# Kernel optimization log

Hardware: AMD Instinct MI355X
Metric: run time of the kernel (lower is better)

## Reference

```python
import jax, jax.numpy as jnp
import numpy as np

C = 1024            # hidden_dim // compression_rate
IN_DIM = 1024
OUT_DIM = 1024
FFT_LEN = C // 2 + 1
CURV = 1e-4         # self.c
EPS = 1e-7
LN_EPS = 1e-5


def _mobius_scalar_mul(r, x, c):
    # r (x) x = tanh(r * atanh(sqrt(c)||x||)) * x / (sqrt(c)||x||)
    sqrt_c = jnp.sqrt(c)
    norm = jnp.maximum(jnp.linalg.norm(x, axis=-1, keepdims=True), EPS)
    scn = jnp.clip(sqrt_c * norm, EPS, 1.0 - 1e-5)
    return jnp.tanh(r * jnp.arctanh(scn)) * x / (sqrt_c * norm)


def _mobius_add(x, y, c):
    x2 = jnp.sum(x * x, axis=-1, keepdims=True)
    y2 = jnp.sum(y * y, axis=-1, keepdims=True)
    xy = jnp.sum(x * y, axis=-1, keepdims=True)
    num = (1.0 + 2.0 * c * xy + c * y2) * x + (1.0 - c * x2) * y
    den = 1.0 + 2.0 * c * xy + (c * c) * x2 * y2
    return num / jnp.maximum(den, EPS)


def _poincare_ball_layer(u, v, c, t):
    # geodesic-style interpolation: ((1-t) (x) u) (+) (t (x) v)
    return _mobius_add(_mobius_scalar_mul(1.0 - t, u, c),
                       _mobius_scalar_mul(t, v, c), c)


def setup_inputs() -> dict:
    key = jax.random.key(0)
    k_x, k_p, k_d = jax.random.split(key, 3)
    std = 0.02
    x = jax.random.normal(k_x, (4, 2048, IN_DIM), dtype=jnp.float32)
    proj_w = jax.random.normal(k_p, (C, IN_DIM), dtype=jnp.float32) * std
    freq_w = jnp.zeros((FFT_LEN,), dtype=jnp.float32)
    t = jnp.float32(0.3)
    ln_g = jnp.ones((C,), dtype=jnp.float32)
    ln_b = jnp.zeros((C,), dtype=jnp.float32)
    down_w = jax.random.normal(k_d, (OUT_DIM, C), dtype=jnp.float32) * std
    scale = jnp.float32(1.0)
    return {"x": x, "proj_w": proj_w, "ln_g": ln_g, "ln_b": ln_b,
            "freq_w": freq_w, "t": t, "down_w": down_w, "scale": scale}


def reference(x, proj_w, ln_g, ln_b, freq_w, t, down_w, scale):
    B, L, _ = x.shape
    # non-sep branch (hidden_dim > in_dim): silu(Linear(x))
    comp = jax.nn.silu(jnp.einsum('bli,ci->blc', x, proj_w))
    mu = jnp.mean(comp, axis=-1, keepdims=True)
    var = jnp.var(comp, axis=-1, keepdims=True)
    comp = (comp - mu) * jax.lax.rsqrt(var + LN_EPS) * ln_g + ln_b
    comp = comp.reshape(-1, C)                     # [B*L, C]
    Xf = jnp.fft.rfft(comp, axis=1)                # [B*L, C//2+1]
    w = jax.nn.softmax(freq_w)[None, :]
    flat = jnp.fft.irfft(Xf * w, n=C, axis=1)
    flat = jnp.nan_to_num(flat)
    shift = jnp.nan_to_num(t * flat)
    hyp = jnp.nan_to_num(_poincare_ball_layer(flat, shift, CURV, t))
    hyp = hyp.reshape(B, L, C)
    return jnp.einsum('blc,oc->blo', hyp, down_w) * scale
```

## Files before the change

kernel.cpp:

```cpp
#include <hip/hip_runtime.h>
#include <math.h>

typedef float f32x4 __attribute__((ext_vector_type(4)));
typedef __bf16 bf16x8 __attribute__((ext_vector_type(8)));

__device__ __forceinline__ unsigned short f2bf(float f) {
  unsigned u = __float_as_uint(f);
  unsigned r = (u + 0x7fffu + ((u >> 16) & 1u)) >> 16;
  return (unsigned short)r;
}
__device__ __forceinline__ float bf2f(unsigned short h) {
  return __uint_as_float(((unsigned)h) << 16);
}

__device__ __forceinline__ float blk_sum(float v, float* red, int tid) {
  #pragma unroll
  for (int o = 32; o; o >>= 1) v += __shfl_down(v, o);
  __syncthreads();
  if ((tid & 63) == 0) red[tid >> 6] = v;
  __syncthreads();
  return red[0] + red[1] + red[2] + red[3];
}

__global__ __launch_bounds__(256) void k_s(const float* __restrict__ fw,
                                           float* __restrict__ s) {
  __shared__ float wsh[513];
  __shared__ float red[4];
  int tid = threadIdx.x;
  float m = -1e30f;
  for (int i = tid; i < 513; i += 256) m = fmaxf(m, fw[i]);
  #pragma unroll
  for (int o = 32; o; o >>= 1) m = fmaxf(m, __shfl_down(m, o));
  if ((tid & 63) == 0) red[tid >> 6] = m;
  __syncthreads();
  m = fmaxf(fmaxf(red[0], red[1]), fmaxf(red[2], red[3]));
  float sum = 0.f;
  for (int i = tid; i < 513; i += 256) {
    float e = expf(fw[i] - m);
    wsh[i] = e;
    sum += e;
  }
  sum = blk_sum(sum, red, tid);
  float inv = 1.f / sum;

  int gid = blockIdx.x * 256 + tid;
  int d = gid >> 3;
  int chunk = gid & 7;
  float acc = 0.f;
  for (int f = 1 + chunk; f < 512; f += 8) {
    int p = (f * d) & 1023;
    acc += wsh[f] * __cosf(6.283185307179586f * (float)p * (1.f / 1024.f));
  }
  acc += __shfl_xor(acc, 1);
  acc += __shfl_xor(acc, 2);
  acc += __shfl_xor(acc, 4);
  if (chunk == 0) {
    float tot = wsh[0] + ((d & 1) ? -wsh[512] : wsh[512]) + 2.f * acc;
    s[d] = tot * inv * (1.f / 1024.f);
  }
}

__global__ __launch_bounds__(256) void k_prep(const float* __restrict__ x,
                                              const float* __restrict__ pw,
                                              const float* __restrict__ dw,
                                              const float* __restrict__ s,
                                              unsigned short* __restrict__ xb,
                                              unsigned short* __restrict__ pwb,
                                              unsigned short* __restrict__ dwb,
                                              unsigned short* __restrict__ Sb) {
  int b = blockIdx.x;
  int tid = threadIdx.x;
  if (b < 8192) {
    int i = b * 256 + tid;
    float4 v = ((const float4*)x)[i];
    ushort4 o;
    o.x = f2bf(v.x); o.y = f2bf(v.y); o.z = f2bf(v.z); o.w = f2bf(v.w);
    ((ushort4*)xb)[i] = o;
  } else if (b < 9216) {
    int i = (b - 8192) * 256 + tid;
    float4 v = ((const float4*)pw)[i];
    ushort4 o;
    o.x = f2bf(v.x); o.y = f2bf(v.y); o.z = f2bf(v.z); o.w = f2bf(v.w);
    ((ushort4*)pwb)[i] = o;
  } else if (b < 10240) {
    int i = (b - 9216) * 256 + tid;
    float4 v = ((const float4*)dw)[i];
    ushort4 o;
    o.x = f2bf(v.x); o.y = f2bf(v.y); o.z = f2bf(v.z); o.w = f2bf(v.w);
    ((ushort4*)dwb)[i] = o;
  } else {
    int idx = (b - 10240) * 256 + tid;
    int n = idx >> 8;
    int k0 = (idx & 255) * 4;
    ushort4 o;
    o.x = f2bf(s[(k0 + 0 - n) & 1023]);
    o.y = f2bf(s[(k0 + 1 - n) & 1023]);
    o.z = f2bf(s[(k0 + 2 - n) & 1023]);
    o.w = f2bf(s[(k0 + 3 - n) & 1023]);
    ((ushort4*)Sb)[idx] = o;
  }
}

__device__ __forceinline__ void gemm_body(const unsigned short* __restrict__ A,
                                          const unsigned short* __restrict__ B,
                                          int bm, int bn, int tid,
                                          char* AsB, char* BsB,
                                          f32x4 acc[4][4]) {
  const int lane = tid & 63;
  const int wave = tid >> 6;
  const int mhalf = (wave & 1) * 64;
  const int nhalf = (wave >> 1) * 64;
  const int ar = tid >> 3;
  const int ac = (((tid & 7) ^ (ar & 7))) * 8;
  const unsigned short* Abase = A + (size_t)(bm + ar) * 1024 + ac;
  const unsigned short* Bbase = B + (size_t)(bn + ar) * 1024 + ac;
  const int mrow = lane & 15;
  const int kq = lane >> 4;
  const int sw = mrow & 7;

  for (int kt = 0; kt < 16; ++kt) {
    const int k0 = kt * 64;
    #pragma unroll
    for (int r = 0; r < 4; ++r) {
      __builtin_amdgcn_global_load_lds(
          (const __attribute__((address_space(1))) void*)(Abase + (size_t)(r * 32) * 1024 + k0),
          (__attribute__((address_space(3))) void*)(AsB + r * 4096 + wave * 1024), 16, 0, 0);
      __builtin_amdgcn_global_load_lds(
          (const __attribute__((address_space(1))) void*)(Bbase + (size_t)(r * 32) * 1024 + k0),
          (__attribute__((address_space(3))) void*)(BsB + r * 4096 + wave * 1024), 16, 0, 0);
    }
    __syncthreads();
    #pragma unroll
    for (int kc = 0; kc < 2; ++kc) {
      const int chunk = (kc << 2) | kq;
      bf16x8 af[4], bfr[4];
      #pragma unroll
      for (int mt = 0; mt < 4; ++mt)
        af[mt] = *(const bf16x8*)(AsB + (mhalf + mt * 16 + mrow) * 128 + ((chunk ^ sw) << 4));
      #pragma unroll
      for (int nt = 0; nt < 4; ++nt)
        bfr[nt] = *(const bf16x8*)(BsB + (nhalf + nt * 16 + mrow) * 128 + ((chunk ^ sw) << 4));
      #pragma unroll
      for (int mt = 0; mt < 4; ++mt)
        #pragma unroll
        for (int nt = 0; nt < 4; ++nt)
          acc[mt][nt] = __builtin_amdgcn_mfma_f32_16x16x32_bf16(af[mt], bfr[nt], acc[mt][nt], 0, 0, 0);
    }
    __syncthreads();
  }
}

__global__ __launch_bounds__(256) void k_gemm1w2(const unsigned short* __restrict__ xb,
                                                 const unsigned short* __restrict__ pwb,
                                                 const unsigned short* __restrict__ dwb,
                                                 const unsigned short* __restrict__ Sb,
                                                 unsigned short* __restrict__ comp,
                                                 unsigned short* __restrict__ W2) {
  __shared__ __align__(16) unsigned short As[128 * 64];
  __shared__ __align__(16) unsigned short Bs[128 * 64];
  const int tid = threadIdx.x;
  const int lane = tid & 63;
  const int wave = tid >> 6;

  if (blockIdx.x < 256) {
    const int bm = ((int)blockIdx.x >> 4) * 64;
    const int bn = ((int)blockIdx.x & 15) * 64;
    const int wm = wave & 1;
    const int wn = wave >> 1;
    f32x4 acc[2][2] = {};
    const int ar = tid >> 3;
    const int ac = (((tid & 7) ^ (ar & 7))) * 8;
    const unsigned short* Abase = dwb + (size_t)(bm + ar) * 1024 + ac;
    const unsigned short* Bbase = Sb + (size_t)(bn + ar) * 1024 + ac;
    char* AsB = (char*)As;
    char* BsB = (char*)Bs;
    const int mrow = lane & 15;
    const int kq = lane >> 4;
    const int sw = mrow & 7;
    for (int kt = 0; kt < 16; ++kt) {
      const int k0 = kt * 64;
      #pragma unroll
      for (int r = 0; r < 2; ++r) {
        __builtin_amdgcn_global_load_lds(
            (const __attribute__((address_space(1))) void*)(Abase + (size_t)(r * 32) * 1024 + k0),
            (__attribute__((address_space(3))) void*)(AsB + r * 4096 + wave * 1024), 16, 0, 0);
        __builtin_amdgcn_global_load_lds(
            (const __attribute__((address_space(1))) void*)(Bbase + (size_t)(r * 32) * 1024 + k0),
            (__attribute__((address_space(3))) void*)(BsB + r * 4096 + wave * 1024), 16, 0, 0);
      }
      __syncthreads();
      #pragma unroll
      for (int kc = 0; kc < 2; ++kc) {
        const int chunk = (kc << 2) | kq;
        bf16x8 af[2], bfr[2];
        #pragma unroll
        for (int mt = 0; mt < 2; ++mt)
          af[mt] = *(const bf16x8*)(AsB + (wm * 32 + mt * 16 + mrow) * 128 + ((chunk ^ sw) << 4));
        #pragma unroll
        for (int nt = 0; nt < 2; ++nt)
          bfr[nt] = *(const bf16x8*)(BsB + (wn * 32 + nt * 16 + mrow) * 128 + ((chunk ^ sw) << 4));
        #pragma unroll
        for (int mt = 0; mt < 2; ++mt)
          #pragma unroll
          for (int nt = 0; nt < 2; ++nt)
            acc[mt][nt] = __builtin_amdgcn_mfma_f32_16x16x32_bf16(af[mt], bfr[nt], acc[mt][nt], 0, 0, 0);
      }
      __syncthreads();
    }
    const int col = bn + wn * 32 + (lane & 15);
    const int rbase = bm + wm * 32 + (lane >> 4) * 4;
    #pragma unroll
    for (int mt = 0; mt < 2; ++mt)
      #pragma unroll
      for (int nt = 0; nt < 2; ++nt)
        #pragma unroll
        for (int r = 0; r < 4; ++r) {
          int row = rbase + mt * 16 + r;
          W2[(size_t)row * 1024 + (col + nt * 16)] = f2bf(acc[mt][nt][r]);
        }
    return;
  }

  const int gid = blockIdx.x - 256;
  const int xcd = gid & 7;
  const int j = gid >> 3;
  const int ntile = j & 7;
  const int bmIdx = xcd + 8 * (j >> 3);
  const int bm = bmIdx * 128;
  const int bn = ntile * 128;
  f32x4 acc[4][4] = {};
  gemm_body(xb, pwb, bm, bn, tid, (char*)As, (char*)Bs, acc);

  const int col = bn + (wave >> 1) * 64 + (lane & 15);
  const int rbase = bm + (wave & 1) * 64 + (lane >> 4) * 4;
  #pragma unroll
  for (int mt = 0; mt < 4; ++mt)
    #pragma unroll
    for (int r = 0; r < 4; ++r) {
      const int row = rbase + mt * 16 + r;
      #pragma unroll
      for (int nt = 0; nt < 4; ++nt) {
        float v = acc[mt][nt][r];
        comp[(size_t)row * 1024 + (col + nt * 16)] = f2bf(v / (1.f + expf(-v)));
      }
    }
}

__global__ __launch_bounds__(256) void k_ln(unsigned short* __restrict__ comp,
                                            const float* __restrict__ ln_g,
                                            const float* __restrict__ ln_b,
                                            float* __restrict__ u2) {
  __shared__ float red[4];
  const int tid = threadIdx.x;
  const size_t rowoff = (size_t)blockIdx.x * 1024;
  if (tid == 0) u2[blockIdx.x] = 0.f;
  ushort4 cv = ((const ushort4*)(comp + rowoff))[tid];
  float x0 = bf2f(cv.x), x1 = bf2f(cv.y), x2 = bf2f(cv.z), x3 = bf2f(cv.w);
  float mu = blk_sum(x0 + x1 + x2 + x3, red, tid) * (1.f / 1024.f);
  float d0 = x0 - mu, d1 = x1 - mu, d2 = x2 - mu, d3 = x3 - mu;
  float var = blk_sum(d0 * d0 + d1 * d1 + d2 * d2 + d3 * d3, red, tid) * (1.f / 1024.f);
  float inv = rsqrtf(var + 1e-5f);
  float4 g = ((const float4*)ln_g)[tid];
  float4 b = ((const float4*)ln_b)[tid];
  ushort4 o;
  o.x = f2bf(d0 * inv * g.x + b.x);
  o.y = f2bf(d1 * inv * g.y + b.y);
  o.z = f2bf(d2 * inv * g.z + b.z);
  o.w = f2bf(d3 * inv * g.w + b.w);
  ((ushort4*)(comp + rowoff))[tid] = o;
}

__device__ __forceinline__ float gamma_from_u2(float U2, float tv) {
  const float sc = 0.01f;
  const float c = 1e-4f;
  float nrm = sqrtf(U2);
  float nu = fmaxf(nrm, 1e-7f);
  float su = fminf(fmaxf(sc * nu, 1e-7f), 1.f - 1e-5f);
  float Af = tanhf((1.f - tv) * atanhf(su)) / (sc * nu);
  float nvn = fmaxf(fabsf(tv) * nrm, 1e-7f);
  float svv = fminf(fmaxf(sc * nvn, 1e-7f), 1.f - 1e-5f);
  float Bf = tv * tanhf(tv * atanhf(svv)) / (sc * nvn);
  float x2s = Af * Af * U2, y2s = Bf * Bf * U2, xys = Af * Bf * U2;
  float numc = (1.f + 2.f * c * xys + c * y2s) * Af + (1.f - c * x2s) * Bf;
  float den = fmaxf(1.f + 2.f * c * xys + c * c * x2s * y2s, 1e-7f);
  return numc / den;
}

__global__ __launch_bounds__(256) void k_gemm23(const unsigned short* __restrict__ comp,
                                                const unsigned short* __restrict__ Sb,
                                                const unsigned short* __restrict__ W2,
                                                unsigned short* __restrict__ raw,
                                                float* __restrict__ u2) {
  __shared__ __align__(16) unsigned short As[128 * 64];
  __shared__ __align__(16) unsigned short Bs[128 * 64];
  const int tid = threadIdx.x;
  const int lane = tid & 63;
  const int wave = tid >> 6;
  const int xcd = blockIdx.x & 7;
  const int j = blockIdx.x >> 3;
  const int ntile = j & 15;
  const int bmIdx = xcd + 8 * (j >> 4);
  const int bm = bmIdx * 128;
  const bool isU2 = (ntile < 8);
  const int bn = (ntile & 7) * 128;
  const unsigned short* B = isU2 ? Sb : W2;
  f32x4 acc[4][4] = {};
  gemm_body(comp, B, bm, bn, tid, (char*)As, (char*)Bs, acc);

  const int col = bn + (wave >> 1) * 64 + (lane & 15);
  const int rbase = bm + (wave & 1) * 64 + (lane >> 4) * 4;
  #pragma unroll
  for (int mt = 0; mt < 4; ++mt)
    #pragma unroll
    for (int r = 0; r < 4; ++r) {
      const int row = rbase + mt * 16 + r;
      if (isU2) {
        float v0 = acc[mt][0][r], v1 = acc[mt][1][r], v2 = acc[mt][2][r], v3 = acc[mt][3][r];
        float ssq = v0 * v0 + v1 * v1 + v2 * v2 + v3 * v3;
        ssq += __shfl_xor(ssq, 1);
        ssq += __shfl_xor(ssq, 2);
        ssq += __shfl_xor(ssq, 4);
        ssq += __shfl_xor(ssq, 8);
        if ((lane & 15) == 0) atomicAdd(&u2[row], ssq);
      } else {
        #pragma unroll
        for (int nt = 0; nt < 4; ++nt)
          raw[(size_t)row * 1024 + (col + nt * 16)] = f2bf(acc[mt][nt][r]);
      }
    }
}

__global__ __launch_bounds__(256) void k_out(const unsigned short* __restrict__ raw,
                                             const float* __restrict__ u2,
                                             const float* __restrict__ t_ptr,
                                             const float* __restrict__ scale_ptr,
                                             float* __restrict__ out) {
  __shared__ float gs;
  const int tid = threadIdx.x;
  const int row = blockIdx.x;
  if (tid == 0) gs = gamma_from_u2(u2[row], t_ptr[0]) * scale_ptr[0];
  __syncthreads();
  const float g = gs;
  ushort4 rv = ((const ushort4*)(raw + (size_t)row * 1024))[tid];
  float4 o;
  o.x = bf2f(rv.x) * g;
  o.y = bf2f(rv.y) * g;
  o.z = bf2f(rv.z) * g;
  o.w = bf2f(rv.w) * g;
  ((float4*)(out + (size_t)row * 1024))[tid] = o;
}

extern "C" void kernel_launch(void* const* d_in, const int* in_sizes, int n_in,
                              void* d_out, int out_size, void* d_ws, size_t ws_size,
                              hipStream_t stream) {
  const float* x      = (const float*)d_in[0];
  const float* proj_w = (const float*)d_in[1];
  const float* ln_g   = (const float*)d_in[2];
  const float* ln_b   = (const float*)d_in[3];
  const float* freq_w = (const float*)d_in[4];
  const float* t_p    = (const float*)d_in[5];
  const float* down_w = (const float*)d_in[6];
  const float* scale  = (const float*)d_in[7];

  char* ws = (char*)d_ws;
  unsigned short* xb   = (unsigned short*)ws;
  unsigned short* pwb  = (unsigned short*)(ws + (16u << 20));
  unsigned short* dwb  = (unsigned short*)(ws + (18u << 20));
  unsigned short* comp = (unsigned short*)(ws + (20u << 20));
  unsigned short* Sb   = (unsigned short*)(ws + (36u << 20));
  unsigned short* W2   = (unsigned short*)(ws + (38u << 20));
  float* s_buf         = (float*)(ws + (40u << 20));
  float* u2            = (float*)(ws + (40u << 20) + 8192);
  unsigned short* raw  = xb;

  k_s<<<32, 256, 0, stream>>>(freq_w, s_buf);
  k_prep<<<11264, 256, 0, stream>>>(x, proj_w, down_w, s_buf, xb, pwb, dwb, Sb);
  k_gemm1w2<<<768, 256, 0, stream>>>(xb, pwb, dwb, Sb, comp, W2);
  k_ln<<<8192, 256, 0, stream>>>(comp, ln_g, ln_b, u2);
  k_gemm23<<<1024, 256, 0, stream>>>(comp, Sb, W2, raw, u2);
  k_out<<<8192, 256, 0, stream>>>(raw, u2, t_p, scale, (float*)d_out);
}
```

Before: 205.3 us.

## Fold LayerNorm into GEMM epilogues via row stats and gamma-scaled weights

Removes the standalone LayerNorm kernel. Row sum and sum of squares are now accumulated with atomics in the GEMM1 epilogue, and ln_g/ln_b are folded into the circulant and W2 weight matrices plus per-column correction vectors. The normalization is then applied algebraically in the GEMM2/3 epilogue. This saves a full read-modify-write pass over the bf16 activation tensor, at the cost of more atomics, an extra small kernel and memset, and a variance computed as E[x²]−mu², which is less numerically stable.

```diff
diff --git a/kernel.cpp b/kernel.cpp
--- a/kernel.cpp
+++ b/kernel.cpp
@@ -64,10 +64,15 @@
                                               const float* __restrict__ pw,
                                               const float* __restrict__ dw,
                                               const float* __restrict__ s,
+                                              const float* __restrict__ ln_g,
+                                              const float* __restrict__ ln_b,
                                               unsigned short* __restrict__ xb,
                                               unsigned short* __restrict__ pwb,
                                               unsigned short* __restrict__ dwb,
-                                              unsigned short* __restrict__ Sb) {
+                                              unsigned short* __restrict__ Sg,
+                                              float* __restrict__ Gs,
+                                              float* __restrict__ Bs2) {
+  __shared__ float red[4];
   int b = blockIdx.x;
   int tid = threadIdx.x;
   if (b < 8192) {
@@ -88,16 +93,29 @@
     ushort4 o;
     o.x = f2bf(v.x); o.y = f2bf(v.y); o.z = f2bf(v.z); o.w = f2bf(v.w);
     ((ushort4*)dwb)[i] = o;
-  } else {
+  } else if (b < 11264) {
     int idx = (b - 10240) * 256 + tid;
     int n = idx >> 8;
     int k0 = (idx & 255) * 4;
+    float4 gv = ((const float4*)ln_g)[idx & 255];
     ushort4 o;
-    o.x = f2bf(s[(k0 + 0 - n) & 1023]);
-    o.y = f2bf(s[(k0 + 1 - n) & 1023]);
-    o.z = f2bf(s[(k0 + 2 - n) & 1023]);
-    o.w = f2bf(s[(k0 + 3 - n) & 1023]);
-    ((ushort4*)Sb)[idx] = o;
+    o.x = f2bf(gv.x * s[(k0 + 0 - n) & 1023]);
+    o.y = f2bf(gv.y * s[(k0 + 1 - n) & 1023]);
+    o.z = f2bf(gv.z * s[(k0 + 2 - n) & 1023]);
+    o.w = f2bf(gv.w * s[(k0 + 3 - n) & 1023]);
+    ((ushort4*)Sg)[idx] = o;
+  } else {
+    int n = b - 11264;
+    int k0 = tid * 4;
+    float4 gv = ((const float4*)ln_g)[tid];
+    float4 bv = ((const float4*)ln_b)[tid];
+    float s0 = s[(k0 + 0 - n) & 1023], s1 = s[(k0 + 1 - n) & 1023];
+    float s2 = s[(k0 + 2 - n) & 1023], s3 = s[(k0 + 3 - n) & 1023];
+    float gp = gv.x * s0 + gv.y * s1 + gv.z * s2 + gv.w * s3;
+    float bp = bv.x * s0 + bv.y * s1 + bv.z * s2 + bv.w * s3;
+    gp = blk_sum(gp, red, tid);
+    bp = blk_sum(bp, red, tid);
+    if (tid == 0) { Gs[n] = gp; Bs2[n] = bp; }
   }
 }
 
@@ -153,9 +171,15 @@
 __global__ __launch_bounds__(256) void k_gemm1w2(const unsigned short* __restrict__ xb,
                                                  const unsigned short* __restrict__ pwb,
                                                  const unsigned short* __restrict__ dwb,
-                                                 const unsigned short* __restrict__ Sb,
+                                                 const unsigned short* __restrict__ Sg,
+                                                 const float* __restrict__ ln_g,
+                                                 const float* __restrict__ ln_b,
                                                  unsigned short* __restrict__ comp,
-                                                 unsigned short* __restrict__ W2) {
+                                                 unsigned short* __restrict__ W2g,
+                                                 float* __restrict__ rowsum,
+                                                 float* __restrict__ rowsum2,
+                                                 float* __restrict__ Gw,
+                                                 float* __restrict__ Bw) {
   __shared__ __align__(16) unsigned short As[128 * 64];
   __shared__ __align__(16) unsigned short Bs[128 * 64];
   const int tid = threadIdx.x;
@@ -163,6 +187,7 @@
   const int wave = tid >> 6;
 
   if (blockIdx.x < 256) {
+    const unsigned short* Sc2 = Sg + (size_t)1024 * 1024;
     const int bm = ((int)blockIdx.x >> 4) * 64;
     const int bn = ((int)blockIdx.x & 15) * 64;
     const int wm = wave & 1;
@@ -171,7 +196,7 @@
     const int ar = tid >> 3;
     const int ac = (((tid & 7) ^ (ar & 7))) * 8;
     const unsigned short* Abase = dwb + (size_t)(bm + ar) * 1024 + ac;
-    const unsigned short* Bbase = Sb + (size_t)(bn + ar) * 1024 + ac;
+    const unsigned short* Bbase = Sc2 + (size_t)(bn + ar) * 1024 + ac;
     char* AsB = (char*)As;
     char* BsB = (char*)Bs;
     const int mrow = lane & 15;
@@ -209,15 +234,31 @@
     }
     const int col = bn + wn * 32 + (lane & 15);
     const int rbase = bm + wm * 32 + (lane >> 4) * 4;
+    float gc[2], bc[2];
+    #pragma unroll
+    for (int nt = 0; nt < 2; ++nt) { gc[nt] = ln_g[col + nt * 16]; bc[nt] = ln_b[col + nt * 16]; }
     #pragma unroll
     for (int mt = 0; mt < 2; ++mt)
       #pragma unroll
-      for (int nt = 0; nt < 2; ++nt)
-        #pragma unroll
-        for (int r = 0; r < 4; ++r) {
-          int row = rbase + mt * 16 + r;
-          W2[(size_t)row * 1024 + (col + nt * 16)] = f2bf(acc[mt][nt][r]);
+      for (int r = 0; r < 4; ++r) {
+        int row = rbase + mt * 16 + r;
+        float gwp = 0.f, bwp = 0.f;
+        #pragma unroll
+        for (int nt = 0; nt < 2; ++nt) {
+          float v = acc[mt][nt][r];
+          W2g[(size_t)row * 1024 + (col + nt * 16)] = f2bf(gc[nt] * v);
+          gwp += gc[nt] * v;
+          bwp += bc[nt] * v;
         }
+        gwp += __shfl_xor(gwp, 1); gwp += __shfl_xor(gwp, 2);
+        gwp += __shfl_xor(gwp, 4); gwp += __shfl_xor(gwp, 8);
+        bwp += __shfl_xor(bwp, 1); bwp += __shfl_xor(bwp, 2);
+        bwp += __shfl_xor(bwp, 4); bwp += __shfl_xor(bwp, 8);
+        if ((lane & 15) == 0) {
+          atomicAdd(&Gw[row], gwp);
+          atomicAdd(&Bw[row], bwp);
+        }
+      }
     return;
   }
 
@@ -238,36 +279,24 @@
     #pragma unroll
     for (int r = 0; r < 4; ++r) {
       const int row = rbase + mt * 16 + r;
+      float s1 = 0.f, s2 = 0.f;
       #pragma unroll
       for (int nt = 0; nt < 4; ++nt) {
         float v = acc[mt][nt][r];
-        comp[(size_t)row * 1024 + (col + nt * 16)] = f2bf(v / (1.f + expf(-v)));
+        float sv = v / (1.f + expf(-v));
+        comp[(size_t)row * 1024 + (col + nt * 16)] = f2bf(sv);
+        s1 += sv;
+        s2 += sv * sv;
+      }
+      s1 += __shfl_xor(s1, 1); s1 += __shfl_xor(s1, 2);
+      s1 += __shfl_xor(s1, 4); s1 += __shfl_xor(s1, 8);
+      s2 += __shfl_xor(s2, 1); s2 += __shfl_xor(s2, 2);
+      s2 += __shfl_xor(s2, 4); s2 += __shfl_xor(s2, 8);
+      if ((lane & 15) == 0) {
+        atomicAdd(&rowsum[row], s1);
+        atomicAdd(&rowsum2[row], s2);
       }
     }
-}
-
-__global__ __launch_bounds__(256) void k_ln(unsigned short* __restrict__ comp,
-                                            const float* __restrict__ ln_g,
-                                            const float* __restrict__ ln_b,
-                                            float* __restrict__ u2) {
-  __shared__ float red[4];
-  const int tid = threadIdx.x;
-  const size_t rowoff = (size_t)blockIdx.x * 1024;
-  if (tid == 0) u2[blockIdx.x] = 0.f;
-  ushort4 cv = ((const ushort4*)(comp + rowoff))[tid];
-  float x0 = bf2f(cv.x), x1 = bf2f(cv.y), x2 = bf2f(cv.z), x3 = bf2f(cv.w);
-  float mu = blk_sum(x0 + x1 + x2 + x3, red, tid) * (1.f / 1024.f);
-  float d0 = x0 - mu, d1 = x1 - mu, d2 = x2 - mu, d3 = x3 - mu;
-  float var = blk_sum(d0 * d0 + d1 * d1 + d2 * d2 + d3 * d3, red, tid) * (1.f / 1024.f);
-  float inv = rsqrtf(var + 1e-5f);
-  float4 g = ((const float4*)ln_g)[tid];
-  float4 b = ((const float4*)ln_b)[tid];
-  ushort4 o;
-  o.x = f2bf(d0 * inv * g.x + b.x);
-  o.y = f2bf(d1 * inv * g.y + b.y);
-  o.z = f2bf(d2 * inv * g.z + b.z);
-  o.w = f2bf(d3 * inv * g.w + b.w);
-  ((ushort4*)(comp + rowoff))[tid] = o;
 }
 
 __device__ __forceinline__ float gamma_from_u2(float U2, float tv) {
@@ -287,12 +316,19 @@
 }
 
 __global__ __launch_bounds__(256) void k_gemm23(const unsigned short* __restrict__ comp,
-                                                const unsigned short* __restrict__ Sb,
-                                                const unsigned short* __restrict__ W2,
+                                                const unsigned short* __restrict__ Sg,
+                                                const unsigned short* __restrict__ W2g,
+                                                const float* __restrict__ rowsum,
+                                                const float* __restrict__ rowsum2,
+                                                const float* __restrict__ Gs,
+                                                const float* __restrict__ Bs2,
+                                                const float* __restrict__ Gw,
+                                                const float* __restrict__ Bw,
                                                 unsigned short* __restrict__ raw,
                                                 float* __restrict__ u2) {
   __shared__ __align__(16) unsigned short As[128 * 64];
   __shared__ __align__(16) unsigned short Bs[128 * 64];
+  __shared__ float muS[128], invS[128], GcS[128], BcS[128];
   const int tid = threadIdx.x;
   const int lane = tid & 63;
   const int wave = tid >> 6;
@@ -303,20 +339,40 @@
   const int bm = bmIdx * 128;
   const bool isU2 = (ntile < 8);
   const int bn = (ntile & 7) * 128;
-  const unsigned short* B = isU2 ? Sb : W2;
+  const unsigned short* B = isU2 ? Sg : W2g;
+
+  if (tid < 128) {
+    float mu = rowsum[bm + tid] * (1.f / 1024.f);
+    float ex2 = rowsum2[bm + tid] * (1.f / 1024.f);
+    muS[tid] = mu;
+    invS[tid] = rsqrtf(ex2 - mu * mu + 1e-5f);
+  } else {
+    int c = tid - 128;
+    GcS[c] = isU2 ? Gs[bn + c] : Gw[bn + c];
+    BcS[c] = isU2 ? Bs2[bn + c] : Bw[bn + c];
+  }
+
   f32x4 acc[4][4] = {};
   gemm_body(comp, B, bm, bn, tid, (char*)As, (char*)Bs, acc);
 
-  const int col = bn + (wave >> 1) * 64 + (lane & 15);
-  const int rbase = bm + (wave & 1) * 64 + (lane >> 4) * 4;
+  const int lcol = (wave >> 1) * 64 + (lane & 15);
+  const int lrbase = (wave & 1) * 64 + (lane >> 4) * 4;
   #pragma unroll
   for (int mt = 0; mt < 4; ++mt)
     #pragma unroll
     for (int r = 0; r < 4; ++r) {
-      const int row = rbase + mt * 16 + r;
+      const int lrow = lrbase + mt * 16 + r;
+      const int row = bm + lrow;
+      const float mu = muS[lrow];
+      const float inv = invS[lrow];
       if (isU2) {
-        float v0 = acc[mt][0][r], v1 = acc[mt][1][r], v2 = acc[mt][2][r], v3 = acc[mt][3][r];
-        float ssq = v0 * v0 + v1 * v1 + v2 * v2 + v3 * v3;
+        float ssq = 0.f;
+        #pragma unroll
+        for (int nt = 0; nt < 4; ++nt) {
+          int c = lcol + nt * 16;
+          float v = inv * (acc[mt][nt][r] - mu * GcS[c]) + BcS[c];
+          ssq += v * v;
+        }
         ssq += __shfl_xor(ssq, 1);
         ssq += __shfl_xor(ssq, 2);
         ssq += __shfl_xor(ssq, 4);
@@ -324,8 +380,11 @@
         if ((lane & 15) == 0) atomicAdd(&u2[row], ssq);
       } else {
         #pragma unroll
-        for (int nt = 0; nt < 4; ++nt)
-          raw[(size_t)row * 1024 + (col + nt * 16)] = f2bf(acc[mt][nt][r]);
+        for (int nt = 0; nt < 4; ++nt) {
+          int c = lcol + nt * 16;
+          float v = inv * (acc[mt][nt][r] - mu * GcS[c]) + BcS[c];
+          raw[(size_t)row * 1024 + (bn + c)] = f2bf(v);
+        }
       }
     }
 }
@@ -350,6 +409,19 @@
   ((float4*)(out + (size_t)row * 1024))[tid] = o;
 }
 
+__global__ __launch_bounds__(256) void k_sc2(const float* __restrict__ s,
+                                             unsigned short* __restrict__ Sc2) {
+  int idx = blockIdx.x * 256 + threadIdx.x;
+  int k = idx >> 8;
+  int n0 = (idx & 255) * 4;
+  ushort4 o;
+  o.x = f2bf(s[(n0 + 0 - k) & 1023]);
+  o.y = f2bf(s[(n0 + 1 - k) & 1023]);
+  o.z = f2bf(s[(n0 + 2 - k) & 1023]);
+  o.w = f2bf(s[(n0 + 3 - k) & 1023]);
+  ((ushort4*)Sc2)[idx] = o;
+}
+
 extern "C" void kernel_launch(void* const* d_in, const int* in_sizes, int n_in,
                               void* d_out, int out_size, void* d_ws, size_t ws_size,
                               hipStream_t stream) {
@@ -367,16 +439,28 @@
   unsigned short* pwb  = (unsigned short*)(ws + (16u << 20));
   unsigned short* dwb  = (unsigned short*)(ws + (18u << 20));
   unsigned short* comp = (unsigned short*)(ws + (20u << 20));
-  unsigned short* Sb   = (unsigned short*)(ws + (36u << 20));
-  unsigned short* W2   = (unsigned short*)(ws + (38u << 20));
-  float* s_buf         = (float*)(ws + (40u << 20));
-  float* u2            = (float*)(ws + (40u << 20) + 8192);
-  unsigned short* raw  = xb;
-
+  unsigned short* Sg   = (unsigned short*)(ws + (36u << 20));
+  unsigned short* Sc2  = (unsigned short*)(ws + (38u << 20));
+  unsigned short* W2g  = (unsigned short*)(ws + (40u << 20));
+  float* s_buf         = (float*)(ws + (42u << 20));
+  float* stats         = (float*)(ws + (42u << 20) + 8192);
+  float* rowsum  = stats;
+  float* rowsum2 = stats + 8192;
+  float* u2      = stats + 16384;
+  float* Gw      = stats + 24576;
+  float* Bw      = stats + 25600;
+  float* Gs      = stats + 26624;
+  float* Bs2     = stats + 27648;
+  unsigned short* raw = xb;
+
+  hipMemsetAsync(stats, 0, 28672 * sizeof(float), stream);
   k_s<<<32, 256, 0, stream>>>(freq_w, s_buf);
-  k_prep<<<11264, 256, 0, stream>>>(x, proj_w, down_w, s_buf, xb, pwb, dwb, Sb);
-  k_gemm1w2<<<768, 256, 0, stream>>>(xb, pwb, dwb, Sb, comp, W2);
-  k_ln<<<8192, 256, 0, stream>>>(comp, ln_g, ln_b, u2);
-  k_gemm23<<<1024, 256, 0, stream>>>(comp, Sb, W2, raw, u2);
+  k_prep<<<12288, 256, 0, stream>>>(x, proj_w, down_w, s_buf, ln_g, ln_b,
+                                    xb, pwb, dwb, Sg, Gs, Bs2);
+  k_sc2<<<1024, 256, 0, stream>>>(s_buf, Sc2);
+  k_gemm1w2<<<768, 256, 0, stream>>>(xb, pwb, dwb, Sg, ln_g, ln_b,
+                                     comp, W2g, rowsum, rowsum2, Gw, Bw);
+  k_gemm23<<<1024, 256, 0, stream>>>(comp, Sg, W2g, rowsum, rowsum2,
+                                     Gs, Bs2, Gw, Bw, raw, u2);
   k_out<<<8192, 256, 0, stream>>>(raw, u2, t_p, scale, (float*)d_out);
 }
```

Measured after the change: 205.5 us. Within noise of the previous version (+0.1%).
